# Kernel tuning notes

Hardware: AMD Instinct MI355X
Metric: run time of the kernel (lower is better)

The kernel has to match this reference:

```python
import jax, jax.numpy as jnp
import numpy as np

LN_EPS = 1e-5


def entmax15(z):
    # exact 1.5-entmax over last axis (Peters & Martins sorting algorithm)
    z = z / 2.0
    z = z - jnp.max(z, axis=-1, keepdims=True)  # shift-invariant, for stability
    zs = -jnp.sort(-z, axis=-1)                 # descending sort
    k = jnp.arange(1, z.shape[-1] + 1, dtype=z.dtype)
    mean = jnp.cumsum(zs, axis=-1) / k
    meansq = jnp.cumsum(zs * zs, axis=-1) / k
    ss = k * (meansq - jnp.square(mean))
    delta = (1.0 - ss) / k
    tau = mean - jnp.sqrt(jnp.clip(delta, 0.0))
    support = jnp.sum((tau <= zs).astype(jnp.int32), axis=-1, keepdims=True)
    tau_star = jnp.take_along_axis(tau, support - 1, axis=-1)
    return jnp.square(jnp.clip(z - tau_star, 0.0))


def layernorm_noaffine(v):
    m = jnp.mean(v, axis=-1, keepdims=True)
    var = jnp.mean(jnp.square(v - m), axis=-1, keepdims=True)
    return (v - m) / jnp.sqrt(var + LN_EPS)


def cp_mumoe(x, gate, Win, Wout):
    ones = jnp.ones(x.shape[:-1] + (1,), x.dtype)
    xb = jnp.concatenate([x, ones], axis=-1)
    z = jnp.einsum('btd,dr->btr', xb, Win) * gate  # [b,t,R]
    return jnp.einsum('btr,or->bto', z, Wout)      # [b,t,o]


def setup_inputs() -> dict:
    key = jax.random.key(0)
    ks = jax.random.split(key, 8)
    B, T, D, O, D2, E, R = 8, 2048, 1024, 4096, 1024, 16, 512
    s = lambda k, shape, scale: jax.random.normal(k, shape, jnp.float32) * scale
    return {
        'x': s(ks[0], (B, T, D), 1.0),
        'proj': s(ks[1], (D, E), D ** -0.5),
        'C1': s(ks[2], (E, R), E ** -0.5),
        'Win1': s(ks[3], (D + 1, R), D ** -0.5),
        'Wout1': s(ks[4], (O, R), R ** -0.5),
        'C2': s(ks[5], (E, R), E ** -0.5),
        'Win2': s(ks[6], (O + 1, R), O ** -0.5),
        'Wout2': s(ks[7], (D2, R), R ** -0.5),
    }


def reference(x, proj, C1, Win1, Wout1, C2, Win2, Wout2):
    # expert gating: projection -> LN (no affine) -> 1.5-entmax
    a = entmax15(layernorm_noaffine(jnp.einsum('btd,de->bte', x, proj)))  # [b,t,E]
    # layer 1: CP-decomposed expert mixture (bias folded into input mode)
    g1 = jnp.einsum('bte,er->btr', a, C1)
    h = cp_mumoe(x, g1, Win1, Wout1)
    # GELU + layer 2 reusing the same gate coefficients
    h = jax.nn.gelu(h, approximate=False)
    g2 = jnp.einsum('bte,er->btr', a, C2)
    return cp_mumoe(h, g2, Win2, Wout2)
```

## Files before the change

### kernel.cpp

```cpp
#include <hip/hip_runtime.h>
#include <hip/hip_bf16.h>
#include <math.h>
#include <stdint.h>

typedef unsigned short u16;
typedef __attribute__((ext_vector_type(8))) short bf16x8;
typedef __attribute__((ext_vector_type(4))) float f32x4;
typedef __attribute__((address_space(3))) void* as3_void;
typedef const __attribute__((address_space(1))) void* as1_cvoid;

__device__ inline u16 f2bf(float f) {
    union { float f; unsigned u; } v; v.f = f;
    unsigned r = v.u + 0x7FFFu + ((v.u >> 16) & 1u);
    return (u16)(r >> 16);
}
__device__ inline float bf2f(u16 h) {
    unsigned u = ((unsigned)h) << 16;
    return __builtin_bit_cast(float, u);
}
__device__ inline float gelu_fast(float v) {
    float t = v * fmaf(0.07135702f, v * v, 1.5957691f);
    return v / (1.f + __expf(-t));
}

template<int CTRL, int RM>
__device__ inline float dpp_mov(float v) {
    return __builtin_bit_cast(float, __builtin_amdgcn_update_dpp(
        0, __builtin_bit_cast(int, v), CTRL, RM, 0xf, false));
}
__device__ inline float wave_sum(float v) {
    v += dpp_mov<0x111, 0xf>(v);
    v += dpp_mov<0x112, 0xf>(v);
    v += dpp_mov<0x114, 0xf>(v);
    v += dpp_mov<0x118, 0xf>(v);
    v += dpp_mov<0x142, 0xa>(v);
    v += dpp_mov<0x143, 0xc>(v);
    return v;
}

__global__ __launch_bounds__(256)
void prep_win(const float* __restrict__ W, u16* __restrict__ Wt,
              float* __restrict__ bias, int logD, int R)
{
    int idx = blockIdx.x * 256 + threadIdx.x;
    int D = 1 << logD;
    int total = D * R;
    if (idx < total) {
        int r = idx >> logD;
        int d = idx & (D - 1);
        Wt[idx] = f2bf(W[(size_t)d * R + r]);
    }
    if (idx < R) bias[idx] = W[(size_t)D * R + idx];
}

__global__ __launch_bounds__(256)
void prep_wout(const float* __restrict__ W, u16* __restrict__ Wt, int total)
{
    int idx = blockIdx.x * 256 + threadIdx.x;
    if (idx < total) Wt[idx] = f2bf(W[idx]);
}

__global__ __launch_bounds__(256)
void k1_proj(const float* __restrict__ x, const float* __restrict__ proj,
             u16* __restrict__ xb, float* __restrict__ sbuf, int Ntok)
{
    __shared__ float plt[16 * 1024];
    const int tid = threadIdx.x;
    #pragma unroll
    for (int k = 0; k < 64; ++k) {
        int idx = k * 256 + tid;
        int e = idx & 15, d = idx >> 4;
        plt[e * 1024 + (d ^ (e << 2))] = proj[idx];
    }
    __syncthreads();

    const int lane = tid & 63;
    const int wid = tid >> 6;
    const int t0 = (blockIdx.x * 4 + wid) * 2;
    if (t0 >= Ntok) return;

    float s[16][2];
    #pragma unroll
    for (int e = 0; e < 16; ++e) { s[e][0] = 0.f; s[e][1] = 0.f; }

    #pragma unroll
    for (int j = 0; j < 4; ++j) {
        const int d0 = (j * 64 + lane) * 4;
        float4 xq[2];
        #pragma unroll
        for (int q = 0; q < 2; ++q) {
            xq[q] = *(const float4*)&x[(size_t)(t0 + q) * 1024 + d0];
            short4 h;
            h.x = (short)f2bf(xq[q].x); h.y = (short)f2bf(xq[q].y);
            h.z = (short)f2bf(xq[q].z); h.w = (short)f2bf(xq[q].w);
            *(short4*)&xb[(size_t)(t0 + q) * 1024 + d0] = h;
        }
        #pragma unroll
        for (int e = 0; e < 16; ++e) {
            float4 p = *(const float4*)&plt[e * 1024 + (d0 ^ (e << 2))];
            #pragma unroll
            for (int q = 0; q < 2; ++q) {
                s[e][q] = fmaf(xq[q].x, p.x, s[e][q]);
                s[e][q] = fmaf(xq[q].y, p.y, s[e][q]);
                s[e][q] = fmaf(xq[q].z, p.z, s[e][q]);
                s[e][q] = fmaf(xq[q].w, p.w, s[e][q]);
            }
        }
    }
    #pragma unroll
    for (int e = 0; e < 16; ++e) {
        s[e][0] = wave_sum(s[e][0]);
        s[e][1] = wave_sum(s[e][1]);
    }
    if (lane == 63) {
        #pragma unroll
        for (int q = 0; q < 2; ++q)
            #pragma unroll
            for (int c = 0; c < 4; ++c) {
                float4 o = { s[c * 4 + 0][q], s[c * 4 + 1][q],
                             s[c * 4 + 2][q], s[c * 4 + 3][q] };
                *(float4*)&sbuf[(size_t)(t0 + q) * 16 + c * 4] = o;
            }
    }
}

__global__ __launch_bounds__(256)
void k1_entmax(const float* __restrict__ sbuf, float* __restrict__ abuf, int Ntok)
{
    int t = blockIdx.x * 256 + threadIdx.x;
    if (t >= Ntok) return;
    float s[16];
    #pragma unroll
    for (int c = 0; c < 4; ++c) {
        float4 v = *(const float4*)&sbuf[(size_t)t * 16 + c * 4];
        s[c * 4 + 0] = v.x; s[c * 4 + 1] = v.y; s[c * 4 + 2] = v.z; s[c * 4 + 3] = v.w;
    }
    float mean = 0.f;
    #pragma unroll
    for (int e = 0; e < 16; ++e) mean += s[e];
    mean *= 0.0625f;
    float var = 0.f;
    #pragma unroll
    for (int e = 0; e < 16; ++e) { float d = s[e] - mean; var = fmaf(d, d, var); }
    var *= 0.0625f;
    float rstd = rsqrtf(var + 1e-5f);

    float z[16];
    #pragma unroll
    for (int e = 0; e < 16; ++e) z[e] = (s[e] - mean) * rstd * 0.5f;
    float zmax = z[0];
    #pragma unroll
    for (int e = 1; e < 16; ++e) zmax = fmaxf(zmax, z[e]);
    #pragma unroll
    for (int e = 0; e < 16; ++e) z[e] -= zmax;

    float zs[16];
    #pragma unroll
    for (int e = 0; e < 16; ++e) zs[e] = z[e];
    #pragma unroll
    for (int k = 2; k <= 16; k <<= 1) {
        #pragma unroll
        for (int j = k >> 1; j > 0; j >>= 1) {
            #pragma unroll
            for (int i = 0; i < 16; ++i) {
                int l = i ^ j;
                if (l > i) {
                    float a = zs[i], b = zs[l];
                    bool asc = ((i & k) == 0);
                    bool sw = asc ? (a > b) : (a < b);
                    if (sw) { zs[i] = b; zs[l] = a; }
                }
            }
        }
    }
    float csum = 0.f, csq = 0.f, tau_star = -3.4e38f;
    #pragma unroll
    for (int kk = 1; kk <= 16; ++kk) {
        float v = zs[16 - kk];
        csum += v; csq += v * v;
        float kf = (float)kk;
        float mn = csum / kf;
        float ms = csq / kf;
        float ss = kf * (ms - mn * mn);
        float delta = fmaxf((1.f - ss) / kf, 0.f);
        float tau = mn - sqrtf(delta);
        if (tau <= v) tau_star = tau;
    }
    #pragma unroll
    for (int c = 0; c < 4; ++c) {
        float4 o;
        float p0 = fmaxf(z[c * 4 + 0] - tau_star, 0.f);
        float p1 = fmaxf(z[c * 4 + 1] - tau_star, 0.f);
        float p2 = fmaxf(z[c * 4 + 2] - tau_star, 0.f);
        float p3 = fmaxf(z[c * 4 + 3] - tau_star, 0.f);
        o.x = p0 * p0; o.y = p1 * p1; o.z = p2 * p2; o.w = p3 * p3;
        *(float4*)&abuf[(size_t)t * 16 + c * 4] = o;
    }
}

__global__ __launch_bounds__(256)
void gcompute(const float* __restrict__ abuf, const float* __restrict__ C1,
              const float* __restrict__ C2, u16* __restrict__ g1,
              u16* __restrict__ g2, int Ntok)
{
    const int tid = threadIdx.x;
    const int lane = tid & 63;
    const int t = blockIdx.x * 4 + (tid >> 6);
    if (t >= Ntok) return;
    float a[16];
    #pragma unroll
    for (int c = 0; c < 4; ++c) {
        float4 v = *(const float4*)&abuf[(size_t)t * 16 + c * 4];
        a[c * 4 + 0] = v.x; a[c * 4 + 1] = v.y; a[c * 4 + 2] = v.z; a[c * 4 + 3] = v.w;
    }
    #pragma unroll
    for (int c8 = 0; c8 < 8; ++c8) {
        int col = c8 * 64 + lane;
        float t1 = 0.f, t2 = 0.f;
        #pragma unroll
        for (int e = 0; e < 16; ++e) {
            t1 = fmaf(a[e], C1[e * 512 + col], t1);
            t2 = fmaf(a[e], C2[e * 512 + col], t2);
        }
        g1[(size_t)t * 512 + col] = f2bf(t1);
        g2[(size_t)t * 512 + col] = f2bf(t2);
    }
}

template<int MODE>
__global__ __launch_bounds__(256, 4)
void gemm_bt(const u16* __restrict__ A, const u16* __restrict__ Bt,
             const float* __restrict__ bias, const u16* __restrict__ gmat,
             void* __restrict__ Cout, int M, int Nn, int K, int tilesN)
{
    __shared__ __align__(1024) char smem[32768];
    const int tid = threadIdx.x;
    const int lane = tid & 63;
    const int wid = tid >> 6;

    int bid = blockIdx.x;
    {
        int nwg = gridDim.x;
        if (nwg >= 16) {
            int q = nwg >> 3, r = nwg & 7;
            int xcd = bid & 7, loc = bid >> 3;
            bid = (xcd < r ? xcd * (q + 1) : r * (q + 1) + (xcd - r) * q) + loc;
        }
    }
    const int m0 = (bid / tilesN) * 128;
    const int n0 = (bid % tilesN) * 128;
    const int wm = (wid >> 1) * 64;
    const int wn = (wid & 1) * 64;

    f32x4 acc[4][4];
    #pragma unroll
    for (int i = 0; i < 4; ++i)
        #pragma unroll
        for (int j = 0; j < 4; ++j) acc[i][j] = (f32x4){0.f, 0.f, 0.f, 0.f};

    const int nsteps = K >> 6;
    for (int ks = 0; ks < nsteps; ++ks) {
        const int k0 = ks << 6;
        #pragma unroll
        for (int i = 0; i < 4; ++i) {
            int q = (wid * 4 + i) * 64 + lane;
            int row = q >> 3;
            int c = (q & 7) ^ (row & 7);
            __builtin_amdgcn_global_load_lds(
                (as1_cvoid)(A + (size_t)(m0 + row) * K + k0 + c * 8),
                (as3_void)&smem[(wid * 4 + i) * 1024], 16, 0, 0);
        }
        #pragma unroll
        for (int i = 0; i < 4; ++i) {
            int q = (wid * 4 + i) * 64 + lane;
            int row = q >> 3;
            int c = (q & 7) ^ (row & 7);
            __builtin_amdgcn_global_load_lds(
                (as1_cvoid)(Bt + (size_t)(n0 + row) * K + k0 + c * 8),
                (as3_void)&smem[16384 + (wid * 4 + i) * 1024], 16, 0, 0);
        }
        __syncthreads();
        #pragma unroll
        for (int kk = 0; kk < 2; ++kk) {
            bf16x8 af[4], bfr[4];
            const int slot = kk * 4 + (lane >> 4);
            #pragma unroll
            for (int i = 0; i < 4; ++i) {
                int row = wm + i * 16 + (lane & 15);
                af[i] = *(const bf16x8*)
                    &smem[row * 128 + ((slot ^ (row & 7)) << 4)];
            }
            #pragma unroll
            for (int j = 0; j < 4; ++j) {
                int row = wn + j * 16 + (lane & 15);
                bfr[j] = *(const bf16x8*)
                    &smem[16384 + row * 128 + ((slot ^ (row & 7)) << 4)];
            }
            #pragma unroll
            for (int i = 0; i < 4; ++i)
                #pragma unroll
                for (int j = 0; j < 4; ++j)
                    acc[i][j] = __builtin_amdgcn_mfma_f32_16x16x32_bf16(
                        af[i], bfr[j], acc[i][j], 0, 0, 0);
        }
        __syncthreads();
    }

    const int cl = lane & 15;
    const int rq = (lane >> 4) * 4;
    #pragma unroll
    for (int i = 0; i < 4; ++i) {
        #pragma unroll
        for (int j = 0; j < 4; ++j) {
            int col = n0 + wn + j * 16 + cl;
            float bv = (MODE == 1) ? bias[col] : 0.f;
            #pragma unroll
            for (int r = 0; r < 4; ++r) {
                int row = m0 + wm + i * 16 + rq + r;
                float v = acc[i][j][r];
                if (MODE == 0) {
                    ((u16*)Cout)[(size_t)row * Nn + col] = f2bf(gelu_fast(v));
                } else if (MODE == 1) {
                    v = (v + bv) * bf2f(gmat[(size_t)row * Nn + col]);
                    ((u16*)Cout)[(size_t)row * Nn + col] = f2bf(v);
                } else {
                    ((float*)Cout)[(size_t)row * Nn + col] = v;
                }
            }
        }
    }
}

extern "C" void kernel_launch(void* const* d_in, const int* in_sizes, int n_in,
                              void* d_out, int out_size, void* d_ws, size_t ws_size,
                              hipStream_t stream)
{
    const float* x     = (const float*)d_in[0];
    const float* proj  = (const float*)d_in[1];
    const float* C1    = (const float*)d_in[2];
    const float* Win1  = (const float*)d_in[3];
    const float* Wout1 = (const float*)d_in[4];
    const float* C2    = (const float*)d_in[5];
    const float* Win2  = (const float*)d_in[6];
    const float* Wout2 = (const float*)d_in[7];

    const int D = 1024, O = 4096, R = 512, D2 = 1024;
    const int Ntok = in_sizes[0] / D;

    char* ws = (char*)d_ws;
    size_t off = 0;
    auto alloc = [&](size_t bytes) -> void* {
        void* p = ws + off;
        off += (bytes + 255) & ~(size_t)255;
        return p;
    };
    u16*   z1  = (u16*)  alloc((size_t)Ntok * R * 2);
    u16*   z2  = (u16*)  alloc((size_t)Ntok * R * 2);
    u16*   w1o = (u16*)  alloc((size_t)O * R * 2);
    u16*   w2t = (u16*)  alloc((size_t)R * O * 2);
    u16*   w2o = (u16*)  alloc((size_t)D2 * R * 2);
    float* b1  = (float*)alloc(R * 4);
    float* b2  = (float*)alloc(R * 4);
    size_t persist_end = off;

    u16*   xb   = (u16*)  alloc((size_t)Ntok * D * 2);
    u16*   w1t  = (u16*)  alloc((size_t)R * D * 2);
    float* sbuf = (float*)alloc((size_t)Ntok * 16 * 4);
    float* abuf = (float*)alloc((size_t)Ntok * 16 * 4);

    size_t hAvail = (ws_size > persist_end) ? (ws_size - persist_end) : 0;
    long long chRows = (long long)(hAvail / ((size_t)O * 2));
    chRows &= ~127LL;
    int CH = (chRows > Ntok) ? Ntok : (int)chRows;
    if (CH < 128) CH = 128;
    u16* hbuf = (u16*)(ws + persist_end);

    u16* g1 = z1;
    u16* g2 = z2;

    prep_win <<<(D * R + 255) / 256, 256, 0, stream>>>(Win1, w1t, b1, 10, R);
    prep_win <<<(O * R + 255) / 256, 256, 0, stream>>>(Win2, w2t, b2, 12, R);
    prep_wout<<<(O * R + 255) / 256, 256, 0, stream>>>(Wout1, w1o, O * R);
    prep_wout<<<(D2 * R + 255) / 256, 256, 0, stream>>>(Wout2, w2o, D2 * R);

    k1_proj  <<<Ntok / 8, 256, 0, stream>>>(x, proj, xb, sbuf, Ntok);
    k1_entmax<<<(Ntok + 255) / 256, 256, 0, stream>>>(sbuf, abuf, Ntok);
    gcompute <<<(Ntok + 3) / 4, 256, 0, stream>>>(abuf, C1, C2, g1, g2, Ntok);

    gemm_bt<1><<<(Ntok / 128) * (R / 128), 256, 0, stream>>>(
        xb, w1t, b1, g1, z1, Ntok, R, D, R / 128);

    for (int r0 = 0; r0 < Ntok; r0 += CH) {
        int cm = Ntok - r0; if (cm > CH) cm = CH;
        gemm_bt<0><<<(cm / 128) * (O / 128), 256, 0, stream>>>(
            z1 + (size_t)r0 * R, w1o, nullptr, nullptr,
            hbuf, cm, O, R, O / 128);
        gemm_bt<1><<<(cm / 128) * (R / 128), 256, 0, stream>>>(
            hbuf, w2t, b2, g2 + (size_t)r0 * R,
            z2 + (size_t)r0 * R, cm, R, O, R / 128);
    }

    gemm_bt<2><<<(Ntok / 128) * (D2 / 128), 256, 0, stream>>>(
        z2, w2o, nullptr, nullptr, d_out, Ntok, D2, R, D2 / 128);
}
```

Measured before the change: 329.5 us.

## Merge weight prep kernels and remap GEMM tiles by M-rows per XCD

Four weight-conversion launches become one prep_all kernel with hard-coded problem sizes, removing three launches. The GEMM block-to-tile mapping now gives each XCD a contiguous band of M-tile rows when the M-tile count is a multiple of 8, so blocks on the same XCD share A rows in L2. The hidden-buffer chunk size is rounded to multiples of 1024 rows, which keeps chunk tile counts divisible by 8. Hard-coding the sizes makes the prep kernel correct only for this shape.

```diff
diff --git a/kernel.cpp b/kernel.cpp
--- a/kernel.cpp
+++ b/kernel.cpp
@@ -39,25 +39,31 @@
 }
 
 __global__ __launch_bounds__(256)
-void prep_win(const float* __restrict__ W, u16* __restrict__ Wt,
-              float* __restrict__ bias, int logD, int R)
+void prep_all(const float* __restrict__ Win1, const float* __restrict__ Wout1,
+              const float* __restrict__ Win2, const float* __restrict__ Wout2,
+              u16* __restrict__ w1t, u16* __restrict__ w1o,
+              u16* __restrict__ w2t, u16* __restrict__ w2o,
+              float* __restrict__ b1, float* __restrict__ b2)
 {
     int idx = blockIdx.x * 256 + threadIdx.x;
-    int D = 1 << logD;
-    int total = D * R;
-    if (idx < total) {
-        int r = idx >> logD;
-        int d = idx & (D - 1);
-        Wt[idx] = f2bf(W[(size_t)d * R + r]);
-    }
-    if (idx < R) bias[idx] = W[(size_t)D * R + idx];
-}
-
-__global__ __launch_bounds__(256)
-void prep_wout(const float* __restrict__ W, u16* __restrict__ Wt, int total)
-{
-    int idx = blockIdx.x * 256 + threadIdx.x;
-    if (idx < total) Wt[idx] = f2bf(W[idx]);
+    if (idx < 524288) {
+        int r = idx >> 10, d = idx & 1023;
+        w1t[idx] = f2bf(Win1[(size_t)d * 512 + r]);
+    }
+    if (idx < 2097152) {
+        w1o[idx] = f2bf(Wout1[idx]);
+    }
+    if (idx < 2097152) {
+        int r = idx >> 12, o = idx & 4095;
+        w2t[idx] = f2bf(Win2[(size_t)o * 512 + r]);
+    }
+    if (idx < 524288) {
+        w2o[idx] = f2bf(Wout2[idx]);
+    }
+    if (idx < 512) {
+        b1[idx] = Win1[(size_t)1024 * 512 + idx];
+        b2[idx] = Win2[(size_t)4096 * 512 + idx];
+    }
 }
 
 __global__ __launch_bounds__(256)
@@ -238,17 +244,22 @@
     const int lane = tid & 63;
     const int wid = tid >> 6;
 
-    int bid = blockIdx.x;
+    int m_t, n_t;
     {
-        int nwg = gridDim.x;
-        if (nwg >= 16) {
-            int q = nwg >> 3, r = nwg & 7;
+        int bid = blockIdx.x;
+        int Mtiles = gridDim.x / tilesN;
+        if ((Mtiles & 7) == 0) {
             int xcd = bid & 7, loc = bid >> 3;
-            bid = (xcd < r ? xcd * (q + 1) : r * (q + 1) + (xcd - r) * q) + loc;
-        }
-    }
-    const int m0 = (bid / tilesN) * 128;
-    const int n0 = (bid % tilesN) * 128;
+            int lm = loc / tilesN;
+            m_t = xcd * (Mtiles >> 3) + lm;
+            n_t = loc - lm * tilesN;
+        } else {
+            m_t = bid / tilesN;
+            n_t = bid % tilesN;
+        }
+    }
+    const int m0 = m_t * 128;
+    const int n0 = n_t * 128;
     const int wm = (wid >> 1) * 64;
     const int wn = (wid & 1) * 64;
 
@@ -370,18 +381,16 @@
 
     size_t hAvail = (ws_size > persist_end) ? (ws_size - persist_end) : 0;
     long long chRows = (long long)(hAvail / ((size_t)O * 2));
-    chRows &= ~127LL;
+    chRows &= ~1023LL;
     int CH = (chRows > Ntok) ? Ntok : (int)chRows;
-    if (CH < 128) CH = 128;
+    if (CH < 1024) CH = 1024;
     u16* hbuf = (u16*)(ws + persist_end);
 
     u16* g1 = z1;
     u16* g2 = z2;
 
-    prep_win <<<(D * R + 255) / 256, 256, 0, stream>>>(Win1, w1t, b1, 10, R);
-    prep_win <<<(O * R + 255) / 256, 256, 0, stream>>>(Win2, w2t, b2, 12, R);
-    prep_wout<<<(O * R + 255) / 256, 256, 0, stream>>>(Wout1, w1o, O * R);
-    prep_wout<<<(D2 * R + 255) / 256, 256, 0, stream>>>(Wout2, w2o, D2 * R);
+    prep_all<<<(O * R + 255) / 256, 256, 0, stream>>>(
+        Win1, Wout1, Win2, Wout2, w1t, w1o, w2t, w2o, b1, b2);
 
     k1_proj  <<<Ntok / 8, 256, 0, stream>>>(x, proj, xb, sbuf, Ntok);
     k1_entmax<<<(Ntok + 255) / 256, 256, 0, stream>>>(sbuf, abuf, Ntok);
```

Result: no change. 324.2 us (median of 2 runs) (-1.6%).
